# Performance work log

Measured on AMD Instinct MI355X. Metric: run time of the kernel, lower is better.

The kernel has to match this reference:

```python
import jax, jax.numpy as jnp
import numpy as np

D_MODEL = 768
NUM_HEADS = 12
NUM_REG = 4
EPS = 1e-5


def _layernorm(x, g, b):
    mu = jnp.mean(x, axis=-1, keepdims=True)
    var = jnp.mean(jnp.square(x - mu), axis=-1, keepdims=True)
    return (x - mu) * jax.lax.rsqrt(var + EPS) * g + b


def _make_mask(seq_len):
    # True = masked (disallowed), matching torch attn_mask bool semantics.
    r1 = 1 + NUM_REG
    mask = np.ones((seq_len, seq_len), dtype=bool)
    mask[0, :] = False                      # context token attends to all
    mask[1:r1, :] = False                   # register tokens attend to all
    mask[r1:, :r1] = False                  # (not use_input_context_token) == False
    mask[r1:, r1:] = ~np.eye(seq_len - r1, dtype=bool)  # feature tokens: self only
    return jnp.asarray(mask)


def setup_inputs() -> dict:
    key = jax.random.key(0)
    ks = jax.random.split(key, 16)
    B, C, H, W = 8, D_MODEL, 32, 32
    d = D_MODEL
    s = 0.02
    inp = {
        "x": jax.random.normal(ks[0], (B, C, H, W), jnp.float32),
        "context_token": jax.random.normal(ks[1], (B, 1, d), jnp.float32),
        "register_tokens": jax.random.normal(ks[2], (B, NUM_REG, d), jnp.float32),
        "in_proj_w": jax.random.normal(ks[3], (3 * d, d), jnp.float32) * s,
        "in_proj_b": jnp.zeros((3 * d,), jnp.float32),
        "out_w": jax.random.normal(ks[4], (d, d), jnp.float32) * s,
        "out_b": jnp.zeros((d,), jnp.float32),
        "ln1_g": jnp.ones((d,), jnp.float32),
        "ln1_b": jnp.zeros((d,), jnp.float32),
        "ln2_g": jnp.ones((d,), jnp.float32),
        "ln2_b": jnp.zeros((d,), jnp.float32),
        "w1": jax.random.normal(ks[5], (4 * d, d), jnp.float32) * s,
        "b1": jnp.zeros((4 * d,), jnp.float32),
        "w2": jax.random.normal(ks[6], (d, 4 * d), jnp.float32) * s,
        "b2": jnp.zeros((d,), jnp.float32),
    }
    return inp


def reference(x, context_token, register_tokens, in_proj_w, in_proj_b,
              out_w, out_b, ln1_g, ln1_b, ln2_g, ln2_b, w1, b1, w2, b2):
    B, C, H, W = x.shape
    d, nh = D_MODEL, NUM_HEADS
    hd = d // nh
    x_flat = x.reshape(B, C, H * W).transpose(0, 2, 1)          # [B, HW, d]
    tokens = jnp.concatenate([context_token, register_tokens], axis=1)
    xw = _layernorm(jnp.concatenate([tokens, x_flat], axis=1), ln1_g, ln1_b)  # [B, S, d]
    S = xw.shape[1]

    qkv = xw @ in_proj_w.T + in_proj_b                           # [B, S, 3d]
    q, k, v = jnp.split(qkv, 3, axis=-1)
    q = q.reshape(B, S, nh, hd).transpose(0, 2, 1, 3)            # [B, nh, S, hd]
    k = k.reshape(B, S, nh, hd).transpose(0, 2, 1, 3)
    v = v.reshape(B, S, nh, hd).transpose(0, 2, 1, 3)

    scores = jnp.einsum("bhqd,bhkd->bhqk", q, k) / jnp.sqrt(jnp.float32(hd))
    mask = _make_mask(S)
    scores = jnp.where(mask, jnp.float32(-1e9), scores)
    probs = jax.nn.softmax(scores, axis=-1)
    attn = jnp.einsum("bhqk,bhkd->bhqd", probs, v)               # [B, nh, S, hd]
    attn = attn.transpose(0, 2, 1, 3).reshape(B, S, d)
    attn = attn @ out_w.T + out_b

    h1 = attn + xw                                                # residual
    ff = _layernorm(h1, ln2_g, ln2_b)
    ff = jax.nn.gelu(ff @ w1.T + b1, approximate=False) @ w2.T + b2
    out = ff + h1                                                 # [B, S, d]

    r1 = 1 + NUM_REG
    ctx_out = out[:, 0:1, :]
    reg_out = out[:, 1:r1, :]
    feat_out = out[:, r1:, :].transpose(0, 2, 1).reshape(B, C, H, W)
    return feat_out, ctx_out, reg_out
```

## Files before the change

kernel.cpp:

```cpp
#include <hip/hip_runtime.h>
#include <math.h>
#include <stdint.h>

#define SEQ 1029
#define BATCH 8
#define M_TOT (BATCH * SEQ)
#define M_PAD 8320
#define NCHUNK 17

typedef float floatx4 __attribute__((ext_vector_type(4)));
typedef __bf16 bf16x8 __attribute__((ext_vector_type(8)));

__device__ __forceinline__ unsigned short f2bf(float f) {
  union { float f; unsigned u; } v; v.f = f;
  unsigned r = v.u + 0x7fffu + ((v.u >> 16) & 1u);
  return (unsigned short)(r >> 16);
}
__device__ __forceinline__ float bf2f(unsigned short h) {
  union { unsigned u; float f; } v; v.u = ((unsigned)h) << 16;
  return v.f;
}
__device__ __forceinline__ float bf_lo(unsigned u) { union { unsigned x; float f; } v; v.x = u << 16; return v.f; }
__device__ __forceinline__ float bf_hi(unsigned u) { union { unsigned x; float f; } v; v.x = u & 0xffff0000u; return v.f; }

__device__ __forceinline__ float wave_sum(float v) {
#pragma unroll
  for (int off = 32; off > 0; off >>= 1) v += __shfl_xor(v, off, 64);
  return v;
}
__device__ __forceinline__ float wave_max(float v) {
#pragma unroll
  for (int off = 32; off > 0; off >>= 1) v = fmaxf(v, __shfl_xor(v, off, 64));
  return v;
}

__device__ __forceinline__ void gload16(const unsigned short* g, unsigned short* l) {
  __builtin_amdgcn_global_load_lds(
      (const __attribute__((address_space(1))) unsigned int*)g,
      (__attribute__((address_space(3))) unsigned int*)l, 16, 0, 0);
}

#define NQ_QKV 442368
#define NQ_OUT 147456
#define NQ_W1  589824
#define NQ_W2  589824
#define NQ_PAD 8448
__global__ void convert_all(const float4* __restrict__ inw, const float4* __restrict__ outw,
                            const float4* __restrict__ w1, const float4* __restrict__ w2,
                            ushort4* __restrict__ wqkv, ushort4* __restrict__ wout,
                            ushort4* __restrict__ w1b, ushort4* __restrict__ w2b,
                            ushort4* __restrict__ xw_pad, ushort4* __restrict__ attn_pad) {
  const int i = blockIdx.x * 256 + threadIdx.x;
  const float4* src; ushort4* dst; int off;
  if (i < NQ_QKV) { src = inw; dst = wqkv; off = i; }
  else if (i < NQ_QKV + NQ_OUT) { src = outw; dst = wout; off = i - NQ_QKV; }
  else if (i < NQ_QKV + NQ_OUT + NQ_W1) { src = w1; dst = w1b; off = i - NQ_QKV - NQ_OUT; }
  else if (i < NQ_QKV + NQ_OUT + NQ_W1 + NQ_W2) { src = w2; dst = w2b; off = i - NQ_QKV - NQ_OUT - NQ_W1; }
  else {
    const int j = i - (NQ_QKV + NQ_OUT + NQ_W1 + NQ_W2);
    const ushort4 z = {0, 0, 0, 0};
    if (j < NQ_PAD) { xw_pad[j] = z; attn_pad[j] = z; }
    return;
  }
  const float4 v = src[off];
  ushort4 o;
  o.x = f2bf(v.x); o.y = f2bf(v.y); o.z = f2bf(v.z); o.w = f2bf(v.w);
  dst[off] = o;
}
#define NQ_ALL (NQ_QKV + NQ_OUT + NQ_W1 + NQ_W2 + NQ_PAD)

__global__ __launch_bounds__(256) void ln1_feat(const float* __restrict__ x,
                                                const float* __restrict__ g,
                                                const float* __restrict__ bta,
                                                unsigned short* __restrict__ xw) {
  __shared__ float tile[768 * 17];
  const int b = blockIdx.y;
  const int hw0 = blockIdx.x * 16;
  const int t = threadIdx.x;
  const float* xb = x + (size_t)b * 768 * 1024;
  const int cl = t >> 4, hl = t & 15;
  for (int it = 0; it < 48; it++) {
    const int c = it * 16 + cl;
    tile[c * 17 + hl] = xb[(size_t)c * 1024 + hw0 + hl];
  }
  __syncthreads();
  const int wave = t >> 6, lane = t & 63;
  for (int tk = wave; tk < 16; tk += 4) {
    float vals[12], s = 0.f, ss = 0.f;
#pragma unroll
    for (int i = 0; i < 12; i++) {
      const float v = tile[(lane + 64 * i) * 17 + tk];
      vals[i] = v; s += v; ss += v * v;
    }
    s = wave_sum(s); ss = wave_sum(ss);
    const float mu = s * (1.0f / 768.0f);
    const float var = ss * (1.0f / 768.0f) - mu * mu;
    const float rs = rsqrtf(var + 1e-5f);
    const int row = b * SEQ + 5 + hw0 + tk;
    unsigned short* orow = xw + (size_t)row * 768;
#pragma unroll
    for (int i = 0; i < 12; i++) {
      const int c = lane + 64 * i;
      orow[c] = f2bf((vals[i] - mu) * rs * g[c] + bta[c]);
    }
  }
}

__global__ __launch_bounds__(256) void ln1_special(const float* __restrict__ ctx,
                                                   const float* __restrict__ regs,
                                                   const float* __restrict__ g,
                                                   const float* __restrict__ bta,
                                                   unsigned short* __restrict__ xw) {
  const int gw = blockIdx.x * 4 + (threadIdx.x >> 6);
  const int lane = threadIdx.x & 63;
  if (gw >= 40) return;
  const int b = gw / 5, s = gw % 5;
  const float* src = (s == 0) ? (ctx + (size_t)b * 768)
                              : (regs + ((size_t)b * 4 + (s - 1)) * 768);
  float vals[12], sm = 0.f, ss = 0.f;
#pragma unroll
  for (int i = 0; i < 12; i++) {
    const float v = src[lane + 64 * i];
    vals[i] = v; sm += v; ss += v * v;
  }
  sm = wave_sum(sm); ss = wave_sum(ss);
  const float mu = sm * (1.0f / 768.0f);
  const float var = ss * (1.0f / 768.0f) - mu * mu;
  const float rs = rsqrtf(var + 1e-5f);
  unsigned short* orow = xw + (size_t)(b * SEQ + s) * 768;
#pragma unroll
  for (int i = 0; i < 12; i++) {
    const int c = lane + 64 * i;
    orow[c] = f2bf((vals[i] - mu) * rs * g[c] + bta[c]);
  }
}

#define BN 128
#define BK 32

template <int EPI, int K, int N, int MT, int NM, int NN>
__global__ __launch_bounds__(256, 4) void gemm_bt(const unsigned short* __restrict__ A,
                                                  const unsigned short* __restrict__ W,
                                                  const float* __restrict__ bias,
                                                  const unsigned short* __restrict__ residb,
                                                  const float* __restrict__ residf,
                                                  float* __restrict__ outf,
                                                  unsigned short* __restrict__ outb) {
  constexpr int BMt = MT * 32;
  __shared__ alignas(16) unsigned short As[2][BMt * BK];
  __shared__ alignas(16) unsigned short Ws[2][BN * BK];
  const int xcd = blockIdx.x & 7;
  const int slot = blockIdx.x >> 3;
  const int tmIdx = xcd + 8 * (slot / NN);
  const int tn = slot % NN;
  if (tmIdx >= NM) return;
  const int tileM = tmIdx * BMt, tileN = tn * BN;

  const int t = threadIdx.x;
  const int wave = t >> 6, lane = t & 63;
  const int quad = lane >> 4, l16 = lane & 15;
  const int wm = (wave & 1) * (MT * 16), wn = (wave >> 1) * 64;

  const int rl = lane >> 2;
  const int kc8 = ((lane & 3) ^ ((rl >> 1) & 3)) * 8;
  const unsigned short* Ag = A + (size_t)(tileM + wave * 16 + rl) * K;
  const unsigned short* Wg = W + (size_t)(tileN + wave * 16 + rl) * K;
  const int ldst = wave * 512 + lane * 8;

  const int koff = ((quad ^ ((l16 >> 1) & 3)) * 8);

  const floatx4 zero4 = {0.f, 0.f, 0.f, 0.f};
  floatx4 acc[MT][4];
#pragma unroll
  for (int i = 0; i < MT; i++)
#pragma unroll
    for (int j = 0; j < 4; j++) acc[i][j] = zero4;

  auto dma = [&](int k0, int buf) {
    gload16(Ag + k0 + kc8, &As[buf][0] + ldst);
    if constexpr (MT == 4)
      gload16(Ag + (size_t)64 * K + k0 + kc8, &As[buf][0] + ldst + 2048);
    gload16(Wg + k0 + kc8, &Ws[buf][0] + ldst);
    gload16(Wg + (size_t)64 * K + k0 + kc8, &Ws[buf][0] + ldst + 2048);
  };
  auto compute = [&](int buf) {
    bf16x8 af[MT], wf[4];
#pragma unroll
    for (int i = 0; i < MT; i++)
      af[i] = *(const bf16x8*)(&As[buf][0] + (wm + i * 16 + l16) * BK + koff);
#pragma unroll
    for (int j = 0; j < 4; j++)
      wf[j] = *(const bf16x8*)(&Ws[buf][0] + (wn + j * 16 + l16) * BK + koff);
#pragma unroll
    for (int i = 0; i < MT; i++)
#pragma unroll
      for (int j = 0; j < 4; j++)
        acc[i][j] = __builtin_amdgcn_mfma_f32_16x16x32_bf16(af[i], wf[j], acc[i][j], 0, 0, 0);
  };

  dma(0, 0);
#pragma unroll 1
  for (int k0 = 0; k0 < K; k0 += 2 * BK) {
    __syncthreads();
    if (k0 + BK < K) dma(k0 + BK, 1);
    compute(0);
    __syncthreads();
    if (k0 + 2 * BK < K) dma(k0 + 2 * BK, 0);
    compute(1);
  }

#pragma unroll
  for (int i = 0; i < MT; i++) {
    const int mbase = tileM + wm + i * 16 + quad * 4;
#pragma unroll
    for (int j = 0; j < 4; j++) {
      const int n = tileN + wn + j * 16 + l16;
      const float bv = bias[n];
#pragma unroll
      for (int r = 0; r < 4; r++) {
        const size_t idx = (size_t)(mbase + r) * N + n;
        float v = acc[i][j][r] + bv;
        if constexpr (EPI == 0) {
          outb[idx] = f2bf(v);
        } else if constexpr (EPI == 1) {
          outf[idx] = v + bf2f(residb[idx]);
        } else if constexpr (EPI == 2) {
          v = 0.5f * v * (1.0f + erff(v * 0.70710678118654752f));
          outb[idx] = f2bf(v);
        } else {
          outf[idx] = v + residf[idx];
        }
      }
    }
  }
}

__global__ __launch_bounds__(256) void attn_feat(const unsigned short* __restrict__ qkv,
                                                 unsigned short* __restrict__ attn) {
  __shared__ float kk[5][64];
  __shared__ float vv[5][64];
  const int b = blockIdx.z, h = blockIdx.y;
  const int t = threadIdx.x;
  const size_t base = (size_t)b * SEQ;
  for (int i = t; i < 320; i += 256) {
    const int j = i >> 6, dd = i & 63;
    const size_t rb = (base + j) * 2304 + (size_t)h * 64 + dd;
    kk[j][dd] = bf2f(qkv[rb + 768]);
    vv[j][dd] = bf2f(qkv[rb + 1536]);
  }
  __syncthreads();
  const int wave = t >> 6, lane = t & 63;
  const int s = 5 + blockIdx.x * 4 + wave;
  const size_t row = (base + s) * 2304 + (size_t)h * 64;
  const float q = bf2f(qkv[row + lane]);
  const float kself = bf2f(qkv[row + 768 + lane]);
  const float vself = bf2f(qkv[row + 1536 + lane]);
  float sc[6];
#pragma unroll
  for (int j = 0; j < 5; j++) sc[j] = wave_sum(q * kk[j][lane]) * 0.125f;
  sc[5] = wave_sum(q * kself) * 0.125f;
  float mx = sc[0];
#pragma unroll
  for (int j = 1; j < 6; j++) mx = fmaxf(mx, sc[j]);
  float den = 0.f, e[6];
#pragma unroll
  for (int j = 0; j < 6; j++) { e[j] = expf(sc[j] - mx); den += e[j]; }
  const float inv = 1.0f / den;
  float o = 0.f;
#pragma unroll
  for (int j = 0; j < 5; j++) o += e[j] * vv[j][lane];
  o += e[5] * vself;
  attn[(base + s) * 768 + (size_t)h * 64 + lane] = f2bf(o * inv);
}

__global__ __launch_bounds__(256) void attn_part(const unsigned short* __restrict__ qkv,
                                                 float* __restrict__ part) {
  __shared__ float qs[5][64];
  __shared__ float sc[5][64];
  __shared__ float mArr[5], lArr[5];
  __shared__ float og[4][320];
  const int c = blockIdx.x, h = blockIdx.y, b = blockIdx.z;
  const int t = threadIdx.x;
  const size_t base = (size_t)b * SEQ;
  const int kbase = (c < 16) ? (5 + 64 * c) : 0;
  const int nvalid = (c < 16) ? 64 : 5;

  for (int i = t; i < 320; i += 256)
    qs[i >> 6][i & 63] = bf2f(qkv[(base + (i >> 6)) * 2304 + (size_t)h * 64 + (i & 63)]);
  __syncthreads();

  const int keyloc = t >> 2, dc = t & 3;
  const int key = kbase + keyloc;
  const unsigned short* krow = qkv + (base + key) * 2304 + 768 + (size_t)h * 64;
  const uint4 k0 = *(const uint4*)(krow + dc * 8);
  const uint4 k1 = *(const uint4*)(krow + dc * 8 + 32);
  float kf[16];
  {
    const unsigned ku[8] = {k0.x, k0.y, k0.z, k0.w, k1.x, k1.y, k1.z, k1.w};
#pragma unroll
    for (int j = 0; j < 8; j++) { kf[2 * j] = bf_lo(ku[j]); kf[2 * j + 1] = bf_hi(ku[j]); }
  }
#pragma unroll
  for (int q = 0; q < 5; q++) {
    const float* qp = qs[q];
    float d0 = 0.f;
#pragma unroll
    for (int j = 0; j < 8; j++) d0 += qp[dc * 8 + j] * kf[j];
#pragma unroll
    for (int j = 0; j < 8; j++) d0 += qp[dc * 8 + 32 + j] * kf[8 + j];
    d0 += __shfl_xor(d0, 1, 64);
    d0 += __shfl_xor(d0, 2, 64);
    if (dc == 0) sc[q][keyloc] = (keyloc < nvalid) ? d0 * 0.125f : -1e30f;
  }
  __syncthreads();

  const int wave = t >> 6, lane = t & 63;
  for (int q = wave; q < 5; q += 4) {
    const float v = sc[q][lane];
    const float m = wave_max(v);
    const float e = expf(v - m);
    sc[q][lane] = e;
    const float l = wave_sum(e);
    if (lane == 0) { mArr[q] = m; lArr[q] = l; }
  }
  __syncthreads();

  const int d = t & 63, g = t >> 6;
  float o[5] = {0.f, 0.f, 0.f, 0.f, 0.f};
  for (int i = 0; i < 16; i++) {
    const int kl = g * 16 + i;
    const float v = bf2f(qkv[(base + kbase + kl) * 2304 + 1536 + (size_t)h * 64 + d]);
#pragma unroll
    for (int q = 0; q < 5; q++) o[q] += sc[q][kl] * v;
  }
#pragma unroll
  for (int q = 0; q < 5; q++) og[g][q * 64 + d] = o[q];
  __syncthreads();

  float* pw = part + (size_t)((b * 12 + h) * NCHUNK + c) * 5 * 66;
  for (int i = t; i < 320; i += 256) {
    const int q = i >> 6, dd = i & 63;
    pw[q * 66 + 2 + dd] = og[0][i] + og[1][i] + og[2][i] + og[3][i];
    if (dd == 0) { pw[q * 66] = mArr[q]; pw[q * 66 + 1] = lArr[q]; }
  }
}

__global__ __launch_bounds__(64) void attn_comb(const float* __restrict__ part,
                                                unsigned short* __restrict__ attn) {
  const int qi = blockIdx.x, h = blockIdx.y, b = blockIdx.z;
  const int d = threadIdx.x;
  float M = -3e38f, L = 0.f, o = 0.f;
  for (int c = 0; c < NCHUNK; c++) {
    const float* p = part + ((size_t)((b * 12 + h) * NCHUNK + c) * 5 + qi) * 66;
    const float mc = p[0], lc = p[1], oc = p[2 + d];
    if (mc > M) {
      const float s = expf(M - mc);
      L = L * s + lc; o = o * s + oc; M = mc;
    } else {
      const float w = expf(mc - M);
      L += lc * w; o += oc * w;
    }
  }
  attn[((size_t)b * SEQ + qi) * 768 + (size_t)h * 64 + d] = f2bf(o / L);
}

__global__ __launch_bounds__(256) void ln2_kernel(const float* __restrict__ h1,
                                                  const float* __restrict__ g,
                                                  const float* __restrict__ bta,
                                                  unsigned short* __restrict__ out) {
  const int row = blockIdx.x * 4 + (threadIdx.x >> 6);
  const int lane = threadIdx.x & 63;
  const float* r = h1 + (size_t)row * 768;
  float vals[12], sm = 0.f, ss = 0.f;
#pragma unroll
  for (int i = 0; i < 12; i++) {
    const float v = r[lane + 64 * i];
    vals[i] = v; sm += v; ss += v * v;
  }
  sm = wave_sum(sm); ss = wave_sum(ss);
  const float mu = sm * (1.0f / 768.0f);
  const float var = ss * (1.0f / 768.0f) - mu * mu;
  const float rs = rsqrtf(var + 1e-5f);
  unsigned short* orow = out + (size_t)row * 768;
#pragma unroll
  for (int i = 0; i < 12; i++) {
    const int c = lane + 64 * i;
    orow[c] = f2bf((vals[i] - mu) * rs * g[c] + bta[c]);
  }
}

__global__ __launch_bounds__(256) void scatter_all(const float* __restrict__ outb,
                                                   float* __restrict__ dout) {
  const int t = threadIdx.x;
  const int b = blockIdx.z;
  if (blockIdx.x == 24) {
    const int i = (b * 32 + blockIdx.y) * 256 + t;
    if (i >= 40 * 768) return;
    const int rowi = i / 768, c = i % 768;
    const int bb = rowi / 5, s = rowi % 5;
    const float v = outb[(size_t)(bb * SEQ + s) * 768 + c];
    if (s == 0) dout[6291456 + (size_t)bb * 768 + c] = v;
    else dout[6291456 + 6144 + ((size_t)bb * 4 + (s - 1)) * 768 + c] = v;
    return;
  }
  __shared__ float tl[32][33];
  const int hw0 = blockIdx.y * 32, c0 = blockIdx.x * 32;
  const int i = t >> 5, j = t & 31;
#pragma unroll
  for (int r = 0; r < 4; r++) {
    const int hwi = i + r * 8;
    tl[hwi][j] = outb[(size_t)(b * SEQ + 5 + hw0 + hwi) * 768 + c0 + j];
  }
  __syncthreads();
#pragma unroll
  for (int r = 0; r < 4; r++) {
    const int ci = i + r * 8;
    dout[(size_t)b * 768 * 1024 + (size_t)(c0 + ci) * 1024 + hw0 + j] = tl[j][ci];
  }
}

extern "C" void kernel_launch(void* const* d_in, const int* in_sizes, int n_in,
                              void* d_out, int out_size, void* d_ws, size_t ws_size,
                              hipStream_t stream) {
  const float* x    = (const float*)d_in[0];
  const float* ctx  = (const float*)d_in[1];
  const float* regs = (const float*)d_in[2];
  const float* inw  = (const float*)d_in[3];
  const float* inb  = (const float*)d_in[4];
  const float* outw = (const float*)d_in[5];
  const float* outbi= (const float*)d_in[6];
  const float* ln1g = (const float*)d_in[7];
  const float* ln1b = (const float*)d_in[8];
  const float* ln2g = (const float*)d_in[9];
  const float* ln2b = (const float*)d_in[10];
  const float* w1   = (const float*)d_in[11];
  const float* b1   = (const float*)d_in[12];
  const float* w2   = (const float*)d_in[13];
  const float* b2   = (const float*)d_in[14];

  char* ws = (char*)d_ws;
  unsigned short* wqkv_b = (unsigned short*)(ws + 0);
  unsigned short* wout_b = (unsigned short*)(ws + 3538944);
  unsigned short* w1_b   = (unsigned short*)(ws + 4718592);
  unsigned short* w2_b   = (unsigned short*)(ws + 9437184);
  unsigned short* xw_b   = (unsigned short*)(ws + 14155776);
  unsigned short* ln2o_b = (unsigned short*)(ws + 26935296);
  float*          h1_f   = (float*)(ws + 39714816);
  unsigned short* qkv_b  = (unsigned short*)(ws + 65273856);
  unsigned short* attn_b = (unsigned short*)(ws + 103612416);
  float*          out_f  = (float*)(ws + 14155776);
  unsigned short* ffm_b  = (unsigned short*)(ws + 65273856);
  float*          part_f = (float*)(ws + 39714816);
  float* dout = (float*)d_out;

  convert_all<<<(NQ_ALL + 255) / 256, 256, 0, stream>>>(
      (const float4*)inw, (const float4*)outw, (const float4*)w1, (const float4*)w2,
      (ushort4*)wqkv_b, (ushort4*)wout_b, (ushort4*)w1_b, (ushort4*)w2_b,
      (ushort4*)(xw_b + (size_t)M_TOT * 768), (ushort4*)(attn_b + (size_t)M_TOT * 768));

  ln1_feat<<<dim3(64, 8), 256, 0, stream>>>(x, ln1g, ln1b, xw_b);
  ln1_special<<<10, 256, 0, stream>>>(ctx, regs, ln1g, ln1b, xw_b);

  gemm_bt<0, 768, 2304, 4, 65, 18><<<8 * 9 * 18, 256, 0, stream>>>(
      xw_b, wqkv_b, inb, nullptr, nullptr, nullptr, qkv_b);

  attn_feat<<<dim3(256, 12, 8), 256, 0, stream>>>(qkv_b, attn_b);
  attn_part<<<dim3(NCHUNK, 12, 8), 256, 0, stream>>>(qkv_b, part_f);
  attn_comb<<<dim3(5, 12, 8), 64, 0, stream>>>(part_f, attn_b);

  gemm_bt<1, 768, 768, 2, 130, 6><<<8 * 17 * 6, 256, 0, stream>>>(
      attn_b, wout_b, outbi, xw_b, nullptr, h1_f, nullptr);

  ln2_kernel<<<M_PAD / 4, 256, 0, stream>>>(h1_f, ln2g, ln2b, ln2o_b);

  gemm_bt<2, 768, 3072, 4, 65, 24><<<8 * 9 * 24, 256, 0, stream>>>(
      ln2o_b, w1_b, b1, nullptr, nullptr, nullptr, ffm_b);

  gemm_bt<3, 3072, 768, 2, 130, 6><<<8 * 17 * 6, 256, 0, stream>>>(
      ffm_b, w2_b, b2, nullptr, h1_f, out_f, nullptr);

  scatter_all<<<dim3(25, 32, 8), 256, 0, stream>>>(out_f, dout);
}
```

Measured before the change: 428.3 us.

## Replace direct-to-LDS loads with register-staged multi-stage GEMM prefetch pipeline

The GEMM kernel no longer uses global_load_lds DMA. It prefetches A/W tiles into registers two or three k-tiles ahead, writes them to a double-buffered LDS, and syncs with a single LDS-count wait plus barrier per k-step. The main loop is unrolled by six so the register-stage indices stay static. The aim is to hide global-load latency behind more MFMA work. The cost is extra VGPR pressure, so the minimum occupancy for the MT==4 variant drops from 4 to 3 blocks per CU.

Result: slower. 1.020 ms (+138.1%).

```diff
diff --git a/kernel.cpp b/kernel.cpp
--- a/kernel.cpp
+++ b/kernel.cpp
@@ -34,10 +34,9 @@
   return v;
 }
 
-__device__ __forceinline__ void gload16(const unsigned short* g, unsigned short* l) {
-  __builtin_amdgcn_global_load_lds(
-      (const __attribute__((address_space(1))) unsigned int*)g,
-      (__attribute__((address_space(3))) unsigned int*)l, 16, 0, 0);
+__device__ __forceinline__ void lgkm0_barrier() {
+  __builtin_amdgcn_s_waitcnt(0xc07f);
+  __builtin_amdgcn_s_barrier();
 }
 
 #define NQ_QKV 442368
@@ -139,16 +138,23 @@
 #define BK 32
 
 template <int EPI, int K, int N, int MT, int NM, int NN>
-__global__ __launch_bounds__(256, 4) void gemm_bt(const unsigned short* __restrict__ A,
-                                                  const unsigned short* __restrict__ W,
-                                                  const float* __restrict__ bias,
-                                                  const unsigned short* __restrict__ residb,
-                                                  const float* __restrict__ residf,
-                                                  float* __restrict__ outf,
-                                                  unsigned short* __restrict__ outb) {
+__global__ __launch_bounds__(256, (MT == 4) ? 3 : 4)
+void gemm_bt(const unsigned short* __restrict__ A,
+             const unsigned short* __restrict__ W,
+             const float* __restrict__ bias,
+             const unsigned short* __restrict__ residb,
+             const float* __restrict__ residf,
+             float* __restrict__ outf,
+             unsigned short* __restrict__ outb) {
   constexpr int BMt = MT * 32;
+  constexpr int GA = BMt / 64 ? BMt / 64 : 1;
+  constexpr int GW = 2;
+  constexpr int D = (MT == 4) ? 2 : 3;
+  constexpr int NK = K / BK;
+
   __shared__ alignas(16) unsigned short As[2][BMt * BK];
   __shared__ alignas(16) unsigned short Ws[2][BN * BK];
+
   const int xcd = blockIdx.x & 7;
   const int slot = blockIdx.x >> 3;
   const int tmIdx = xcd + 8 * (slot / NN);
@@ -162,10 +168,11 @@
   const int wm = (wave & 1) * (MT * 16), wn = (wave >> 1) * 64;
 
   const int rl = lane >> 2;
-  const int kc8 = ((lane & 3) ^ ((rl >> 1) & 3)) * 8;
-  const unsigned short* Ag = A + (size_t)(tileM + wave * 16 + rl) * K;
-  const unsigned short* Wg = W + (size_t)(tileN + wave * 16 + rl) * K;
-  const int ldst = wave * 512 + lane * 8;
+  const int csrc = (lane & 3) * 8;
+  const int dchunk = ((lane & 3) ^ ((rl >> 1) & 3)) * 8;
+  const unsigned short* Agp = A + (size_t)(tileM + wave * 16 + rl) * K + csrc;
+  const unsigned short* Wgp = W + (size_t)(tileN + wave * 16 + rl) * K + csrc;
+  const int lrow = (wave * 16 + rl) * BK + dchunk;
 
   const int koff = ((quad ^ ((l16 >> 1) & 3)) * 8);
 
@@ -176,12 +183,22 @@
 #pragma unroll
     for (int j = 0; j < 4; j++) acc[i][j] = zero4;
 
-  auto dma = [&](int k0, int buf) {
-    gload16(Ag + k0 + kc8, &As[buf][0] + ldst);
-    if constexpr (MT == 4)
-      gload16(Ag + (size_t)64 * K + k0 + kc8, &As[buf][0] + ldst + 2048);
-    gload16(Wg + k0 + kc8, &Ws[buf][0] + ldst);
-    gload16(Wg + (size_t)64 * K + k0 + kc8, &Ws[buf][0] + ldst + 2048);
+  uint4 ra[D][GA], rw[D][GW];
+  auto loadG = [&](int tile, int s) {
+#pragma unroll
+    for (int g = 0; g < GA; g++)
+      ra[s][g] = *(const uint4*)(Agp + (size_t)tile * BK + (size_t)g * 64 * K);
+#pragma unroll
+    for (int g = 0; g < GW; g++)
+      rw[s][g] = *(const uint4*)(Wgp + (size_t)tile * BK + (size_t)g * 64 * K);
+  };
+  auto writeL = [&](int s, int buf) {
+#pragma unroll
+    for (int g = 0; g < GA; g++)
+      *(uint4*)(&As[buf][0] + lrow + g * 64 * BK) = ra[s][g];
+#pragma unroll
+    for (int g = 0; g < GW; g++)
+      *(uint4*)(&Ws[buf][0] + lrow + g * 64 * BK) = rw[s][g];
   };
   auto compute = [&](int buf) {
     bf16x8 af[MT], wf[4];
@@ -198,15 +215,22 @@
         acc[i][j] = __builtin_amdgcn_mfma_f32_16x16x32_bf16(af[i], wf[j], acc[i][j], 0, 0, 0);
   };
 
-  dma(0, 0);
+  loadG(0, 0);
+  writeL(0, 0);
+  loadG(1, 1 % D);
+  if (D == 3) loadG(2, 2);
+  lgkm0_barrier();
+
 #pragma unroll 1
-  for (int k0 = 0; k0 < K; k0 += 2 * BK) {
-    __syncthreads();
-    if (k0 + BK < K) dma(k0 + BK, 1);
-    compute(0);
-    __syncthreads();
-    if (k0 + 2 * BK < K) dma(k0 + 2 * BK, 0);
-    compute(1);
+  for (int trip = 0; trip < NK / 6; ++trip) {
+#pragma unroll
+    for (int u = 0; u < 6; ++u) {
+      const int k = trip * 6 + u;
+      if (k + D < NK) loadG(k + D, u % D);
+      if (k + 1 < NK) writeL((u + 1) % D, (u + 1) & 1);
+      compute(u & 1);
+      lgkm0_barrier();
+    }
   }
 
 #pragma unroll
```

## Triple-buffer GEMM K-loop with explicit vmcnt waits instead of syncthreads

Applied to the files above, without the earlier changes.

The bf16 MFMA GEMM moves from double to triple buffering in LDS. Global-to-LDS loads are issued two tiles ahead, and each step waits with a precise s_waitcnt vmcnt count plus a raw s_barrier instead of a full __syncthreads. The goal is to hide more global-load latency behind the matrix-core work. In exchange, LDS use per block grows, so launch bounds drop to 3 blocks per CU for the MT=4 variant, which can lower occupancy. The loop assumes K/BK is a multiple of 3, which holds for K = 768 and K = 3072.

New measurement: 431.2 us. About the same (+0.7%).

```diff
diff --git a/kernel.cpp b/kernel.cpp
--- a/kernel.cpp
+++ b/kernel.cpp
@@ -32,6 +32,16 @@
 #pragma unroll
   for (int off = 32; off > 0; off >>= 1) v = fmaxf(v, __shfl_xor(v, off, 64));
   return v;
+}
+
+template <int V> __device__ __forceinline__ void vm_wait();
+template <> __device__ __forceinline__ void vm_wait<0>() { asm volatile("s_waitcnt vmcnt(0)" ::: "memory"); }
+template <> __device__ __forceinline__ void vm_wait<3>() { asm volatile("s_waitcnt vmcnt(3)" ::: "memory"); }
+template <> __device__ __forceinline__ void vm_wait<4>() { asm volatile("s_waitcnt vmcnt(4)" ::: "memory"); }
+template <> __device__ __forceinline__ void vm_wait<6>() { asm volatile("s_waitcnt vmcnt(6)" ::: "memory"); }
+template <> __device__ __forceinline__ void vm_wait<8>() { asm volatile("s_waitcnt vmcnt(8)" ::: "memory"); }
+__device__ __forceinline__ void raw_barrier() {
+  __builtin_amdgcn_s_barrier();
 }
 
 __device__ __forceinline__ void gload16(const unsigned short* g, unsigned short* l) {
@@ -139,16 +149,21 @@
 #define BK 32
 
 template <int EPI, int K, int N, int MT, int NM, int NN>
-__global__ __launch_bounds__(256, 4) void gemm_bt(const unsigned short* __restrict__ A,
-                                                  const unsigned short* __restrict__ W,
-                                                  const float* __restrict__ bias,
-                                                  const unsigned short* __restrict__ residb,
-                                                  const float* __restrict__ residf,
-                                                  float* __restrict__ outf,
-                                                  unsigned short* __restrict__ outb) {
+__global__ __launch_bounds__(256, (MT == 4) ? 3 : 4)
+void gemm_bt(const unsigned short* __restrict__ A,
+             const unsigned short* __restrict__ W,
+             const float* __restrict__ bias,
+             const unsigned short* __restrict__ residb,
+             const float* __restrict__ residf,
+             float* __restrict__ outf,
+             unsigned short* __restrict__ outb) {
   constexpr int BMt = MT * 32;
-  __shared__ alignas(16) unsigned short As[2][BMt * BK];
-  __shared__ alignas(16) unsigned short Ws[2][BN * BK];
+  constexpr int NK = K / BK;
+  constexpr int P = (MT == 4) ? 4 : 3;
+
+  __shared__ alignas(16) unsigned short As[3][BMt * BK];
+  __shared__ alignas(16) unsigned short Ws[3][BN * BK];
+
   const int xcd = blockIdx.x & 7;
   const int slot = blockIdx.x >> 3;
   const int tmIdx = xcd + 8 * (slot / NN);
@@ -176,7 +191,8 @@
 #pragma unroll
     for (int j = 0; j < 4; j++) acc[i][j] = zero4;
 
-  auto dma = [&](int k0, int buf) {
+  auto dma = [&](int kt, int buf) {
+    const int k0 = kt * BK;
     gload16(Ag + k0 + kc8, &As[buf][0] + ldst);
     if constexpr (MT == 4)
       gload16(Ag + (size_t)64 * K + k0 + kc8, &As[buf][0] + ldst + 2048);
@@ -199,14 +215,22 @@
   };
 
   dma(0, 0);
+  dma(1, 1);
+  dma(2, 2);
+
 #pragma unroll 1
-  for (int k0 = 0; k0 < K; k0 += 2 * BK) {
-    __syncthreads();
-    if (k0 + BK < K) dma(k0 + BK, 1);
-    compute(0);
-    __syncthreads();
-    if (k0 + 2 * BK < K) dma(k0 + 2 * BK, 0);
-    compute(1);
+  for (int kb = 0; kb < NK; kb += 3) {
+#pragma unroll
+    for (int u = 0; u < 3; ++u) {
+      const int k = kb + u;
+      if (k + 2 < NK) vm_wait<2 * P>();
+      else if (k + 1 < NK) vm_wait<P>();
+      else vm_wait<0>();
+      raw_barrier();
+      compute(u);
+      raw_barrier();
+      if (k + 3 < NK) dma(k + 3, u);
+    }
   }
 
 #pragma unroll
```
